# Performance work log

Measured on AMD Instinct MI355X. Metric: run time of the kernel, lower is better.

## Reference

```python
import jax, jax.numpy as jnp
import numpy as np

B, T, C = 4, 8192, 1024
H, D = 16, 64  # n_head, head_dim


def setup_inputs() -> dict:
    key = jax.random.key(0)
    ks = jax.random.split(key, 9)
    s = 1.0 / np.sqrt(C)
    return {
        "x": jax.random.normal(ks[0], (B, T, C), jnp.float32),
        "Wq": jax.random.uniform(ks[1], (C, C), jnp.float32, -s, s),
        "bq": jax.random.uniform(ks[2], (C,), jnp.float32, -s, s),
        "Wk": jax.random.uniform(ks[3], (C, C), jnp.float32, -s, s),
        "bk": jax.random.uniform(ks[4], (C,), jnp.float32, -s, s),
        "Wv": jax.random.uniform(ks[5], (C, C), jnp.float32, -s, s),
        "bv": jax.random.uniform(ks[6], (C,), jnp.float32, -s, s),
        "Wp": jax.random.uniform(ks[7], (C, C), jnp.float32, -s, s),
        "bp": jax.random.uniform(ks[8], (C,), jnp.float32, -s, s),
    }


def _heads(t):
    # (B,T,C) -> (B,H,T,D)
    return t.reshape(B, T, H, D).transpose(0, 2, 1, 3)


def reference(x, Wq, bq, Wk, bk, Wv, bv, Wp, bp):
    q = _heads(x @ Wq.T + bq)
    k = _heads(x @ Wk.T + bk)
    v = _heads(x @ Wv.T + bv)
    # attn_type='l1': softmax q,k over feature dim; L1 normalizer
    q = jax.nn.softmax(q, axis=-1)
    k = jax.nn.softmax(k, axis=-1)
    k_sum = k.sum(axis=-2, keepdims=True)               # (B,H,1,D)
    D_inv = 1.0 / (q * k_sum).sum(axis=-1, keepdims=True)  # (B,H,T,1)
    context = jnp.einsum('bhtd,bhte->bhde', k, v)       # (B,H,D,D)
    out = jnp.einsum('bhtd,bhde->bhte', q, context) * D_inv + q
    out = out.transpose(0, 2, 1, 3).reshape(B, T, C)
    return out @ Wp.T + bp
```

## Files before the change

### kernel.cpp

```cpp
#include <hip/hip_runtime.h>
#include <hip/hip_bf16.h>
#include <stdint.h>


#define BT    32768
#define CDIM  1024

using bf16 = __hip_bfloat16;
typedef short  short8   __attribute__((ext_vector_type(8)));
typedef short  short4_t __attribute__((ext_vector_type(4)));
typedef unsigned short ushort4_t __attribute__((ext_vector_type(4)));
typedef float  floatx4  __attribute__((ext_vector_type(4)));

__device__ __forceinline__ float bfbits2f(unsigned short u) {
    union { unsigned int i; float f; } c; c.i = ((unsigned int)u) << 16; return c.f;
}

__device__ __forceinline__ void gld_lds16(const void* g, void* lds) {
    __builtin_amdgcn_global_load_lds(
        (const __attribute__((address_space(1))) uint32_t*)g,
        (__attribute__((address_space(3))) uint32_t*)lds,
        16, 0, 0);
}

__global__ void zero_kernel(float* __restrict__ p) {
    p[(size_t)blockIdx.x * 256 + threadIdx.x] = 0.0f;
}

__global__ void cvt_kernel(const float* __restrict__ x,
                           const float* __restrict__ Wq, const float* __restrict__ Wk,
                           const float* __restrict__ Wv, const float* __restrict__ Wp,
                           bf16* __restrict__ xb, bf16* __restrict__ Wb) {
    const int XF4 = (BT * CDIM) / 4;
    int i = blockIdx.x * 256 + threadIdx.x;
    const float* src; bf16* dst; int off;
    if (i < XF4) { src = x; dst = xb; off = i; }
    else {
        int i2 = i - XF4;
        int wi = i2 >> 18;
        off = i2 & 0x3FFFF;
        src = (wi == 0) ? Wq : (wi == 1) ? Wk : (wi == 2) ? Wv : Wp;
        dst = Wb + (size_t)wi * 1048576;
    }
    float4 f = ((const float4*)src)[off];
    union { bf16 h[4]; short4_t v; } u;
    u.h[0] = __float2bfloat16(f.x); u.h[1] = __float2bfloat16(f.y);
    u.h[2] = __float2bfloat16(f.z); u.h[3] = __float2bfloat16(f.w);
    *(short4_t*)(dst + (size_t)off * 4) = u.v;
}

__global__ __launch_bounds__(256)
void gemm_qkv(const bf16* __restrict__ A, const bf16* __restrict__ Bw,
              const float* __restrict__ bq, const float* __restrict__ bk,
              const float* __restrict__ bv,
              bf16* __restrict__ qb, bf16* __restrict__ kb, bf16* __restrict__ vb) {
    __shared__ bf16 sA[128 * 32];
    __shared__ bf16 sB[128 * 32];
    int tid = threadIdx.x, lane = tid & 63, wv = tid >> 6;
    int bn = blockIdx.x % 24;
    int bm = blockIdx.x / 24;
    const bf16* Ab = A  + (size_t)bm * 128 * CDIM;
    const bf16* Bb = Bw + (size_t)bn * 128 * CDIM;
    int srow = lane >> 2;
    int scol = ((lane & 3) ^ ((lane >> 3) & 3)) * 8;

    floatx4 acc[4][4] = {};
    int quad = lane >> 4, l15 = lane & 15;
    int m0 = (wv & 1) * 64, n0v = (wv >> 1) * 64;
    int rpos = (quad ^ ((l15 >> 1) & 3)) * 8;

    for (int kt = 0; kt < 32; ++kt) {
        int k0 = kt * 32;
        #pragma unroll
        for (int c = 0; c < 2; ++c) {
            int chunk = wv * 2 + c;
            gld_lds16(Ab + (size_t)(chunk * 16 + srow) * CDIM + k0 + scol, &sA[chunk * 512]);
            gld_lds16(Bb + (size_t)(chunk * 16 + srow) * CDIM + k0 + scol, &sB[chunk * 512]);
        }
        __syncthreads();
        short8 af[4], bfr[4];
        #pragma unroll
        for (int i = 0; i < 4; ++i) {
            af[i]  = *(const short8*)&sA[(m0  + i * 16 + l15) * 32 + rpos];
            bfr[i] = *(const short8*)&sB[(n0v + i * 16 + l15) * 32 + rpos];
        }
        #pragma unroll
        for (int i = 0; i < 4; ++i)
            #pragma unroll
            for (int j = 0; j < 4; ++j)
                acc[i][j] = __builtin_amdgcn_mfma_f32_16x16x32_bf16(af[i], bfr[j], acc[i][j], 0, 0, 0);
        __syncthreads();
    }

    int grow0 = bm * 128 + m0;
    int n_abs = bn * 128 + n0v;
    bf16* dst; const float* biasp; int ncol0; bool smax;
    if (n_abs < 1024)      { dst = qb; biasp = bq; ncol0 = n_abs;        smax = true;  }
    else if (n_abs < 2048) { dst = kb; biasp = bk; ncol0 = n_abs - 1024; smax = true;  }
    else                   { dst = vb; biasp = bv; ncol0 = n_abs - 2048; smax = false; }
    float bias4[4];
    #pragma unroll
    for (int j = 0; j < 4; ++j) bias4[j] = biasp[ncol0 + j * 16 + l15];

    #pragma unroll
    for (int i = 0; i < 4; ++i) {
        #pragma unroll
        for (int r = 0; r < 4; ++r) {
            float vals[4];
            #pragma unroll
            for (int j = 0; j < 4; ++j) vals[j] = acc[i][j][r] + bias4[j];
            if (smax) {
                float mx = fmaxf(fmaxf(vals[0], vals[1]), fmaxf(vals[2], vals[3]));
                #pragma unroll
                for (int d = 1; d < 16; d <<= 1) mx = fmaxf(mx, __shfl_xor(mx, d));
                float s = 0.f;
                #pragma unroll
                for (int j = 0; j < 4; ++j) { vals[j] = __expf(vals[j] - mx); s += vals[j]; }
                #pragma unroll
                for (int d = 1; d < 16; d <<= 1) s += __shfl_xor(s, d);
                float rinv = 1.0f / s;
                #pragma unroll
                for (int j = 0; j < 4; ++j) vals[j] *= rinv;
            }
            size_t row = (size_t)(grow0 + i * 16 + quad * 4 + r);
            #pragma unroll
            for (int j = 0; j < 4; ++j)
                dst[row * 1024 + ncol0 + j * 16 + l15] = __float2bfloat16(vals[j]);
        }
    }
}

__global__ __launch_bounds__(256)
void ctx_kernel(const bf16* __restrict__ kbuf, const bf16* __restrict__ vbuf,
                float* __restrict__ ctx, float* __restrict__ ksum) {
    int bid = blockIdx.x;
    int head = bid >> 4, chunk = bid & 15;
    int b = head >> 4, h = head & 15;
    size_t rowbase = (size_t)b * 8192 + (size_t)chunk * 512;
    int coff = h * 64;
    __shared__ bf16 ks[64 * 64];
    __shared__ bf16 vs[64 * 64];
    int tid = threadIdx.x;
    int lrow = tid >> 2, lpart = tid & 3;
    int di = tid >> 4, ei = tid & 15;

    float acc[16];
    #pragma unroll
    for (int i = 0; i < 16; ++i) acc[i] = 0.f;
    float ksv[4] = {0.f, 0.f, 0.f, 0.f};

    size_t gbase = (rowbase + lrow) * 1024 + coff + lpart * 16;
    short8 pk0 = *(const short8*)(kbuf + gbase);
    short8 pk1 = *(const short8*)(kbuf + gbase + 8);
    short8 pv0 = *(const short8*)(vbuf + gbase);
    short8 pv1 = *(const short8*)(vbuf + gbase + 8);

    for (int st = 0; st < 8; ++st) {
        __syncthreads();
        *(short8*)&ks[lrow * 64 + lpart * 16]     = pk0;
        *(short8*)&ks[lrow * 64 + lpart * 16 + 8] = pk1;
        *(short8*)&vs[lrow * 64 + lpart * 16]     = pv0;
        *(short8*)&vs[lrow * 64 + lpart * 16 + 8] = pv1;
        __syncthreads();
        if (st < 7) {
            size_t g = gbase + (size_t)(st + 1) * 64 * 1024;
            pk0 = *(const short8*)(kbuf + g);
            pk1 = *(const short8*)(kbuf + g + 8);
            pv0 = *(const short8*)(vbuf + g);
            pv1 = *(const short8*)(vbuf + g + 8);
        }
        for (int t = 0; t < 64; ++t) {
            ushort4_t ku = *(const ushort4_t*)&ks[t * 64 + di * 4];
            ushort4_t vu = *(const ushort4_t*)&vs[t * 64 + ei * 4];
            float kd[4], ve[4];
            #pragma unroll
            for (int i = 0; i < 4; ++i) { kd[i] = bfbits2f(ku[i]); ve[i] = bfbits2f(vu[i]); }
            #pragma unroll
            for (int i = 0; i < 4; ++i)
                #pragma unroll
                for (int j = 0; j < 4; ++j)
                    acc[i * 4 + j] = fmaf(kd[i], ve[j], acc[i * 4 + j]);
            #pragma unroll
            for (int j = 0; j < 4; ++j) ksv[j] += kd[j];
        }
    }
    float* cptr = ctx + (size_t)head * 4096;
    #pragma unroll
    for (int i = 0; i < 4; ++i)
        #pragma unroll
        for (int j = 0; j < 4; ++j)
            atomicAdd(&cptr[(di * 4 + i) * 64 + ei * 4 + j], acc[i * 4 + j]);
    if (ei == 0) {
        #pragma unroll
        for (int j = 0; j < 4; ++j) atomicAdd(&ksum[head * 64 + di * 4 + j], ksv[j]);
    }
}

#define QS 72
__global__ __launch_bounds__(256)
void attn_kernel(const bf16* __restrict__ qbuf, const float* __restrict__ ctx,
                 const float* __restrict__ ksum, bf16* __restrict__ ab) {
    int bid = blockIdx.x;
    int head = bid >> 7, tb = bid & 127;
    int b = head >> 4, h = head & 15;
    size_t row0 = (size_t)b * 8192 + (size_t)tb * 64;
    int coff = h * 64;
    __shared__ bf16 qs[64 * QS];
    __shared__ bf16 cts[64 * QS];
    __shared__ float ksums[64];
    __shared__ float dinv[64];
    int tid = threadIdx.x, lane = tid & 63, wv = tid >> 6;

    {
        int lrow = tid >> 2, lpart = tid & 3;
        size_t g = (row0 + lrow) * 1024 + coff + lpart * 16;
        short8 q0 = *(const short8*)(qbuf + g);
        short8 q1 = *(const short8*)(qbuf + g + 8);
        *(short8*)&qs[lrow * QS + lpart * 16]     = q0;
        *(short8*)&qs[lrow * QS + lpart * 16 + 8] = q1;
    }
    {
        const float* cp = ctx + (size_t)head * 4096;
        #pragma unroll
        for (int it = 0; it < 4; ++it) {
            int fi = it * 256 + tid;
            int d = fi >> 4, e0 = (fi & 15) * 4;
            float4 f = ((const float4*)cp)[fi];
            cts[(e0 + 0) * QS + d] = __float2bfloat16(f.x);
            cts[(e0 + 1) * QS + d] = __float2bfloat16(f.y);
            cts[(e0 + 2) * QS + d] = __float2bfloat16(f.z);
            cts[(e0 + 3) * QS + d] = __float2bfloat16(f.w);
        }
    }
    if (tid < 64) ksums[tid] = ksum[head * 64 + tid];
    __syncthreads();

    {
        int t = tid >> 2, dg = tid & 3;
        float p = 0.f;
        #pragma unroll
        for (int j = 0; j < 16; ++j)
            p = fmaf(__bfloat162float(qs[t * QS + dg * 16 + j]), ksums[dg * 16 + j], p);
        p += __shfl_xor(p, 1);
        p += __shfl_xor(p, 2);
        if (dg == 0) dinv[t] = 1.0f / p;
    }
    __syncthreads();

    int quad = lane >> 4, l15 = lane & 15;
    int trow0 = wv * 16;
    short8 aF0 = *(const short8*)&qs[(trow0 + l15) * QS + quad * 8];
    short8 aF1 = *(const short8*)&qs[(trow0 + l15) * QS + 32 + quad * 8];
    floatx4 acc[4] = {};
    #pragma unroll
    for (int ni = 0; ni < 4; ++ni) {
        short8 b0 = *(const short8*)&cts[(ni * 16 + l15) * QS + quad * 8];
        short8 b1 = *(const short8*)&cts[(ni * 16 + l15) * QS + 32 + quad * 8];
        acc[ni] = __builtin_amdgcn_mfma_f32_16x16x32_bf16(aF0, b0, acc[ni], 0, 0, 0);
        acc[ni] = __builtin_amdgcn_mfma_f32_16x16x32_bf16(aF1, b1, acc[ni], 0, 0, 0);
    }
    float dv[4];
    #pragma unroll
    for (int r = 0; r < 4; ++r) dv[r] = dinv[trow0 + quad * 4 + r];
    #pragma unroll
    for (int ni = 0; ni < 4; ++ni) {
        #pragma unroll
        for (int r = 0; r < 4; ++r) {
            int row = trow0 + quad * 4 + r;
            int col = ni * 16 + l15;
            float val = acc[ni][r] * dv[r] + __bfloat162float(qs[row * QS + col]);
            ab[(row0 + row) * 1024 + coff + col] = __float2bfloat16(val);
        }
    }
}

__global__ __launch_bounds__(256)
void gemm_out(const bf16* __restrict__ A, const bf16* __restrict__ Bw,
              const float* __restrict__ bp, float* __restrict__ outp) {
    __shared__ bf16 sA[128 * 32];
    __shared__ bf16 sB[128 * 32];
    int tid = threadIdx.x, lane = tid & 63, wv = tid >> 6;
    int bn = blockIdx.x & 7;
    int bm = blockIdx.x >> 3;
    const bf16* Ab = A  + (size_t)bm * 128 * CDIM;
    const bf16* Bb = Bw + (size_t)bn * 128 * CDIM;
    int srow = lane >> 2;
    int scol = ((lane & 3) ^ ((lane >> 3) & 3)) * 8;
    floatx4 acc[4][4] = {};
    int quad = lane >> 4, l15 = lane & 15;
    int m0 = (wv & 1) * 64, n0v = (wv >> 1) * 64;
    int rpos = (quad ^ ((l15 >> 1) & 3)) * 8;

    for (int kt = 0; kt < 32; ++kt) {
        int k0 = kt * 32;
        #pragma unroll
        for (int c = 0; c < 2; ++c) {
            int chunk = wv * 2 + c;
            gld_lds16(Ab + (size_t)(chunk * 16 + srow) * CDIM + k0 + scol, &sA[chunk * 512]);
            gld_lds16(Bb + (size_t)(chunk * 16 + srow) * CDIM + k0 + scol, &sB[chunk * 512]);
        }
        __syncthreads();
        short8 af[4], bfr[4];
        #pragma unroll
        for (int i = 0; i < 4; ++i) {
            af[i]  = *(const short8*)&sA[(m0  + i * 16 + l15) * 32 + rpos];
            bfr[i] = *(const short8*)&sB[(n0v + i * 16 + l15) * 32 + rpos];
        }
        #pragma unroll
        for (int i = 0; i < 4; ++i)
            #pragma unroll
            for (int j = 0; j < 4; ++j)
                acc[i][j] = __builtin_amdgcn_mfma_f32_16x16x32_bf16(af[i], bfr[j], acc[i][j], 0, 0, 0);
        __syncthreads();
    }
    int grow0 = bm * 128 + m0;
    int gcol0 = bn * 128 + n0v;
    float bias4[4];
    #pragma unroll
    for (int j = 0; j < 4; ++j) bias4[j] = bp[gcol0 + j * 16 + l15];
    #pragma unroll
    for (int i = 0; i < 4; ++i)
        #pragma unroll
        for (int r = 0; r < 4; ++r) {
            size_t row = (size_t)(grow0 + i * 16 + quad * 4 + r);
            #pragma unroll
            for (int j = 0; j < 4; ++j)
                outp[row * 1024 + gcol0 + j * 16 + l15] = acc[i][j][r] + bias4[j];
        }
}

extern "C" void kernel_launch(void* const* d_in, const int* in_sizes, int n_in,
                              void* d_out, int out_size, void* d_ws, size_t ws_size,
                              hipStream_t stream) {
    const float* x  = (const float*)d_in[0];
    const float* Wq = (const float*)d_in[1];
    const float* bq = (const float*)d_in[2];
    const float* Wk = (const float*)d_in[3];
    const float* bk = (const float*)d_in[4];
    const float* Wv = (const float*)d_in[5];
    const float* bv = (const float*)d_in[6];
    const float* Wp = (const float*)d_in[7];
    const float* bp = (const float*)d_in[8];
    float* outp = (float*)d_out;

    char* ws = (char*)d_ws;
    bf16*  xb   = (bf16*)(ws);
    bf16*  Wb   = (bf16*)(ws + 67108864);
    bf16*  qb   = (bf16*)(ws + 75497472);
    bf16*  kb   = (bf16*)(ws + 142606336);
    bf16*  vb   = (bf16*)(ws + 209715200);
    float* ctx  = (float*)(ws + 276824064);
    float* ksum = (float*)(ws + 277872640);
    bf16*  ab   = (bf16*)(ws);

    zero_kernel<<<1040, 256, 0, stream>>>(ctx);
    cvt_kernel<<<36864, 256, 0, stream>>>(x, Wq, Wk, Wv, Wp, xb, Wb);
    gemm_qkv<<<6144, 256, 0, stream>>>(xb, Wb, bq, bk, bv, qb, kb, vb);
    ctx_kernel<<<1024, 256, 0, stream>>>(kb, vb, ctx, ksum);
    attn_kernel<<<8192, 256, 0, stream>>>(qb, ctx, ksum, ab);
    gemm_out<<<2048, 256, 0, stream>>>(ab, Wb + (size_t)3072 * 1024, bp, outp);
}
```

Measured before the change: 723.6 us.

## Rewrite QKV and output GEMMs as 256x256 tiles with double-buffered async pipeline

Both GEMMs now use a shared 256x256-tile, 512-thread routine. It double-buffers 64-wide K slices in LDS with direct global-to-LDS loads, interleaves staging with MFMA phases using explicit vmcnt waits and barriers, and raises wave priority around MFMA bursts. The block index is remapped so neighbouring blocks share A/B panels in cache. The aim is to hide global-load latency and raise arithmetic intensity over the old single-buffered 128x128, K=32 loop. In exchange it uses 128KB of LDS and more accumulator registers per block, and the hand-tuned waitcnt counts are fragile.

Result: faster. 691.3 us (-4.5%).

```diff
diff --git a/kernel.cpp b/kernel.cpp
--- a/kernel.cpp
+++ b/kernel.cpp
@@ -49,51 +49,120 @@
     *(short4_t*)(dst + (size_t)off * 4) = u.v;
 }
 
-__global__ __launch_bounds__(256)
+
+__device__ __forceinline__ short8 frag_ld(const bf16* hb, int r, int s4q) {
+    return *(const short8*)(hb + r * 64 + (((s4q) ^ (r & 7)) << 3));
+}
+
+__device__ __forceinline__ void stage_half(const bf16* g, bf16* l, int tid) {
+    int ln = tid & 63, w = tid >> 6;
+    int r = w * 8 + (ln >> 3);
+    int c = ((ln & 7) ^ (ln >> 3)) << 3;
+    gld_lds16(g + (size_t)r * CDIM + c, l + w * 512);
+    gld_lds16(g + (size_t)(r + 64) * CDIM + c, l + 4096 + w * 512);
+}
+
+#define MFMA16(a, b, c) __builtin_amdgcn_mfma_f32_16x16x32_bf16(a, b, c, 0, 0, 0)
+
+__device__ __forceinline__ void pipe256(const bf16* __restrict__ Ab,
+                                        const bf16* __restrict__ Bb,
+                                        bf16* ldsA, bf16* ldsB,
+                                        int tid, floatx4 acc[8][4]) {
+    const int lane = tid & 63;
+    const int wv = tid >> 6;
+    const int quad = lane >> 4, l15 = lane & 15;
+    const int wm = wv >> 2, wn = wv & 3;
+    const int rA0 = wm * 64 + l15;
+    const int rB0 = (wn & 1) * 64 + l15;
+    const bf16* ldsBh = ldsB + (wn >> 1) * 8192;
+    short8 bfr[4][2];
+
+#define STAGE_A(b, h, kt) stage_half(Ab + (size_t)((h) * 128) * CDIM + (kt) * 64, \
+                                     ldsA + (b) * 16384 + (h) * 8192, tid)
+#define STAGE_B(b, h, kt) stage_half(Bb + (size_t)((h) * 128) * CDIM + (kt) * 64, \
+                                     ldsB + (b) * 16384 + (h) * 8192, tid)
+#define VMW(n) asm volatile("s_waitcnt vmcnt(" #n ")" ::: "memory")
+#define VM_NONE
+
+#define QPHASE(BUF, QA, MM, LOADB, STG, VMC) do {                              \
+    const bf16* aH_ = ldsA + (BUF) * 16384 + (QA) * 8192;                      \
+    short8 a00_ = frag_ld(aH_, rA0 + (MM) * 32,      quad);                    \
+    short8 a01_ = frag_ld(aH_, rA0 + (MM) * 32,      4 + quad);                \
+    short8 a10_ = frag_ld(aH_, rA0 + (MM) * 32 + 16, quad);                    \
+    short8 a11_ = frag_ld(aH_, rA0 + (MM) * 32 + 16, 4 + quad);                \
+    if (LOADB) {                                                               \
+        const bf16* bH_ = ldsBh + (BUF) * 16384;                               \
+        _Pragma("unroll")                                                      \
+        for (int j = 0; j < 4; ++j) {                                          \
+            bfr[j][0] = frag_ld(bH_, rB0 + j * 16, quad);                      \
+            bfr[j][1] = frag_ld(bH_, rB0 + j * 16, 4 + quad);                  \
+        }                                                                      \
+    }                                                                          \
+    STG; VMC;                                                                  \
+    __builtin_amdgcn_s_barrier();                                              \
+    asm volatile("s_waitcnt lgkmcnt(0)" ::: "memory");                         \
+    __builtin_amdgcn_s_setprio(1);                                             \
+    _Pragma("unroll")                                                          \
+    for (int j = 0; j < 4; ++j) {                                              \
+        acc[(QA)*4+(MM)*2  ][j] = MFMA16(a00_, bfr[j][0], acc[(QA)*4+(MM)*2  ][j]); \
+        acc[(QA)*4+(MM)*2  ][j] = MFMA16(a01_, bfr[j][1], acc[(QA)*4+(MM)*2  ][j]); \
+        acc[(QA)*4+(MM)*2+1][j] = MFMA16(a10_, bfr[j][0], acc[(QA)*4+(MM)*2+1][j]); \
+        acc[(QA)*4+(MM)*2+1][j] = MFMA16(a11_, bfr[j][1], acc[(QA)*4+(MM)*2+1][j]); \
+    }                                                                          \
+    __builtin_amdgcn_s_setprio(0);                                             \
+    __builtin_amdgcn_s_barrier();                                              \
+} while (0)
+
+    STAGE_B(0, 0, 0); STAGE_B(0, 1, 0); STAGE_A(0, 0, 0); STAGE_A(0, 1, 0);
+    STAGE_B(1, 0, 1); STAGE_B(1, 1, 1); STAGE_A(1, 0, 1);
+    VMW(8);
+    __builtin_amdgcn_s_barrier();
+
+    #pragma unroll 1
+    for (int i = 0; i < 7; ++i) {
+        int t = 2 * i;
+        QPHASE(0, 0, 0, 1, STAGE_A(1, 1, t + 1), VM_NONE);
+        QPHASE(0, 0, 1, 0, STAGE_B(0, 0, t + 2), VMW(10));
+        QPHASE(0, 1, 0, 0, STAGE_B(0, 1, t + 2), VM_NONE);
+        QPHASE(0, 1, 1, 0, STAGE_A(0, 0, t + 2), VMW(8));
+        QPHASE(1, 0, 0, 1, STAGE_A(0, 1, t + 2), VM_NONE);
+        QPHASE(1, 0, 1, 0, STAGE_B(1, 0, t + 3), VMW(10));
+        QPHASE(1, 1, 0, 0, STAGE_B(1, 1, t + 3), VM_NONE);
+        QPHASE(1, 1, 1, 0, STAGE_A(1, 0, t + 3), VMW(8));
+    }
+    QPHASE(0, 0, 0, 1, STAGE_A(1, 1, 15), VM_NONE);
+    QPHASE(0, 0, 1, 0, VM_NONE, VMW(8));
+    QPHASE(0, 1, 0, 0, VM_NONE, VM_NONE);
+    QPHASE(0, 1, 1, 0, VM_NONE, VMW(2));
+    QPHASE(1, 0, 0, 1, VM_NONE, VM_NONE);
+    QPHASE(1, 0, 1, 0, VM_NONE, VMW(0));
+    QPHASE(1, 1, 0, 0, VM_NONE, VM_NONE);
+    QPHASE(1, 1, 1, 0, VM_NONE, VM_NONE);
+
+#undef QPHASE
+#undef STAGE_A
+#undef STAGE_B
+}
+
+__global__ __launch_bounds__(512, 2)
 void gemm_qkv(const bf16* __restrict__ A, const bf16* __restrict__ Bw,
               const float* __restrict__ bq, const float* __restrict__ bk,
               const float* __restrict__ bv,
               bf16* __restrict__ qb, bf16* __restrict__ kb, bf16* __restrict__ vb) {
-    __shared__ bf16 sA[128 * 32];
-    __shared__ bf16 sB[128 * 32];
-    int tid = threadIdx.x, lane = tid & 63, wv = tid >> 6;
-    int bn = blockIdx.x % 24;
-    int bm = blockIdx.x / 24;
-    const bf16* Ab = A  + (size_t)bm * 128 * CDIM;
-    const bf16* Bb = Bw + (size_t)bn * 128 * CDIM;
-    int srow = lane >> 2;
-    int scol = ((lane & 3) ^ ((lane >> 3) & 3)) * 8;
-
-    floatx4 acc[4][4] = {};
-    int quad = lane >> 4, l15 = lane & 15;
-    int m0 = (wv & 1) * 64, n0v = (wv >> 1) * 64;
-    int rpos = (quad ^ ((l15 >> 1) & 3)) * 8;
-
-    for (int kt = 0; kt < 32; ++kt) {
-        int k0 = kt * 32;
-        #pragma unroll
-        for (int c = 0; c < 2; ++c) {
-            int chunk = wv * 2 + c;
-            gld_lds16(Ab + (size_t)(chunk * 16 + srow) * CDIM + k0 + scol, &sA[chunk * 512]);
-            gld_lds16(Bb + (size_t)(chunk * 16 + srow) * CDIM + k0 + scol, &sB[chunk * 512]);
-        }
-        __syncthreads();
-        short8 af[4], bfr[4];
-        #pragma unroll
-        for (int i = 0; i < 4; ++i) {
-            af[i]  = *(const short8*)&sA[(m0  + i * 16 + l15) * 32 + rpos];
-            bfr[i] = *(const short8*)&sB[(n0v + i * 16 + l15) * 32 + rpos];
-        }
-        #pragma unroll
-        for (int i = 0; i < 4; ++i)
-            #pragma unroll
-            for (int j = 0; j < 4; ++j)
-                acc[i][j] = __builtin_amdgcn_mfma_f32_16x16x32_bf16(af[i], bfr[j], acc[i][j], 0, 0, 0);
-        __syncthreads();
-    }
-
-    int grow0 = bm * 128 + m0;
-    int n_abs = bn * 128 + n0v;
+    __shared__ bf16 ldsA[32768];
+    __shared__ bf16 ldsB[32768];
+    int tid = threadIdx.x;
+    int bid = blockIdx.x;
+    int swz = (bid & 7) * 192 + (bid >> 3);
+    int bn = swz % 12, bm = swz / 12;
+
+    floatx4 acc[8][4] = {};
+    pipe256(A + (size_t)bm * 256 * CDIM, Bw + (size_t)bn * 256 * CDIM,
+            ldsA, ldsB, tid, acc);
+
+    int lane = tid & 63, wv = tid >> 6, quad = lane >> 4, l15 = lane & 15;
+    int wm = wv >> 2, wn = wv & 3;
+    int n_abs = bn * 256 + wn * 64;
     bf16* dst; const float* biasp; int ncol0; bool smax;
     if (n_abs < 1024)      { dst = qb; biasp = bq; ncol0 = n_abs;        smax = true;  }
     else if (n_abs < 2048) { dst = kb; biasp = bk; ncol0 = n_abs - 1024; smax = true;  }
@@ -101,9 +170,10 @@
     float bias4[4];
     #pragma unroll
     for (int j = 0; j < 4; ++j) bias4[j] = biasp[ncol0 + j * 16 + l15];
-
-    #pragma unroll
-    for (int i = 0; i < 4; ++i) {
+    size_t row0 = (size_t)bm * 256 + wm * 64;
+
+    #pragma unroll
+    for (int i = 0; i < 8; ++i) {
         #pragma unroll
         for (int r = 0; r < 4; ++r) {
             float vals[4];
@@ -122,7 +192,7 @@
                 #pragma unroll
                 for (int j = 0; j < 4; ++j) vals[j] *= rinv;
             }
-            size_t row = (size_t)(grow0 + i * 16 + quad * 4 + r);
+            size_t row = row0 + ((i >> 2) * 128) + ((i & 3) * 16) + quad * 4 + r;
             #pragma unroll
             for (int j = 0; j < 4; ++j)
                 dst[row * 1024 + ncol0 + j * 16 + l15] = __float2bfloat16(vals[j]);
@@ -274,59 +344,38 @@
     }
 }
 
-__global__ __launch_bounds__(256)
+__global__ __launch_bounds__(512, 2)
 void gemm_out(const bf16* __restrict__ A, const bf16* __restrict__ Bw,
               const float* __restrict__ bp, float* __restrict__ outp) {
-    __shared__ bf16 sA[128 * 32];
-    __shared__ bf16 sB[128 * 32];
-    int tid = threadIdx.x, lane = tid & 63, wv = tid >> 6;
-    int bn = blockIdx.x & 7;
-    int bm = blockIdx.x >> 3;
-    const bf16* Ab = A  + (size_t)bm * 128 * CDIM;
-    const bf16* Bb = Bw + (size_t)bn * 128 * CDIM;
-    int srow = lane >> 2;
-    int scol = ((lane & 3) ^ ((lane >> 3) & 3)) * 8;
-    floatx4 acc[4][4] = {};
-    int quad = lane >> 4, l15 = lane & 15;
-    int m0 = (wv & 1) * 64, n0v = (wv >> 1) * 64;
-    int rpos = (quad ^ ((l15 >> 1) & 3)) * 8;
-
-    for (int kt = 0; kt < 32; ++kt) {
-        int k0 = kt * 32;
-        #pragma unroll
-        for (int c = 0; c < 2; ++c) {
-            int chunk = wv * 2 + c;
-            gld_lds16(Ab + (size_t)(chunk * 16 + srow) * CDIM + k0 + scol, &sA[chunk * 512]);
-            gld_lds16(Bb + (size_t)(chunk * 16 + srow) * CDIM + k0 + scol, &sB[chunk * 512]);
-        }
-        __syncthreads();
-        short8 af[4], bfr[4];
-        #pragma unroll
-        for (int i = 0; i < 4; ++i) {
-            af[i]  = *(const short8*)&sA[(m0  + i * 16 + l15) * 32 + rpos];
-            bfr[i] = *(const short8*)&sB[(n0v + i * 16 + l15) * 32 + rpos];
-        }
-        #pragma unroll
-        for (int i = 0; i < 4; ++i)
-            #pragma unroll
-            for (int j = 0; j < 4; ++j)
-                acc[i][j] = __builtin_amdgcn_mfma_f32_16x16x32_bf16(af[i], bfr[j], acc[i][j], 0, 0, 0);
-        __syncthreads();
-    }
-    int grow0 = bm * 128 + m0;
-    int gcol0 = bn * 128 + n0v;
+    __shared__ bf16 ldsA[32768];
+    __shared__ bf16 ldsB[32768];
+    int tid = threadIdx.x;
+    int bid = blockIdx.x;
+    int swz = (bid & 7) * 64 + (bid >> 3);
+    int bn = swz & 3, bm = swz >> 2;
+
+    floatx4 acc[8][4] = {};
+    pipe256(A + (size_t)bm * 256 * CDIM, Bw + (size_t)bn * 256 * CDIM,
+            ldsA, ldsB, tid, acc);
+
+    int lane = tid & 63, wv = tid >> 6, quad = lane >> 4, l15 = lane & 15;
+    int wm = wv >> 2, wn = wv & 3;
+    int gcol0 = bn * 256 + wn * 64;
     float bias4[4];
     #pragma unroll
     for (int j = 0; j < 4; ++j) bias4[j] = bp[gcol0 + j * 16 + l15];
-    #pragma unroll
-    for (int i = 0; i < 4; ++i)
+    size_t row0 = (size_t)bm * 256 + wm * 64;
+
+    #pragma unroll
+    for (int i = 0; i < 8; ++i) {
         #pragma unroll
         for (int r = 0; r < 4; ++r) {
-            size_t row = (size_t)(grow0 + i * 16 + quad * 4 + r);
+            size_t row = row0 + ((i >> 2) * 128) + ((i & 3) * 16) + quad * 4 + r;
             #pragma unroll
             for (int j = 0; j < 4; ++j)
                 outp[row * 1024 + gcol0 + j * 16 + l15] = acc[i][j][r] + bias4[j];
         }
+    }
 }
 
 extern "C" void kernel_launch(void* const* d_in, const int* in_sizes, int n_in,
@@ -355,8 +404,8 @@
 
     zero_kernel<<<1040, 256, 0, stream>>>(ctx);
     cvt_kernel<<<36864, 256, 0, stream>>>(x, Wq, Wk, Wv, Wp, xb, Wb);
-    gemm_qkv<<<6144, 256, 0, stream>>>(xb, Wb, bq, bk, bv, qb, kb, vb);
+    gemm_qkv<<<1536, 512, 0, stream>>>(xb, Wb, bq, bk, bv, qb, kb, vb);
     ctx_kernel<<<1024, 256, 0, stream>>>(kb, vb, ctx, ksum);
     attn_kernel<<<8192, 256, 0, stream>>>(qb, ctx, ksum, ab);
-    gemm_out<<<2048, 256, 0, stream>>>(ab, Wb + (size_t)3072 * 1024, bp, outp);
-}
+    gemm_out<<<512, 512, 0, stream>>>(ab, Wb + (size_t)3072 * 1024, bp, outp);
+}
```
